# Kernel tuning notes

Hardware: AMD Instinct MI355X
Metric: run time of the kernel (lower is better)

Reference implementation:

```python
import jax, jax.numpy as jnp
import numpy as np

N_ING, N_DIR = 100000, 50000
E = 1000000
H, D = 4, 16          # heads, per-head dim
HID = H * D           # 64
LAT, COND = 32, 8
F_ING, F_DIR = 16, 8
OUT_ING = 16


def _han_edge(x_src, x_dst, att_s, att_d, edge_index, n_dst):
    # HANConv per-edge-type attention message passing.
    src, dst = edge_index[0], edge_index[1]
    a = jax.nn.leaky_relu(
        jnp.einsum('nhd,hd->nh', x_src, att_s)[src]
        + jnp.einsum('nhd,hd->nh', x_dst, att_d)[dst],
        negative_slope=0.2)                               # [E, H]
    amax = jax.ops.segment_max(a, dst, num_segments=n_dst)
    ex = jnp.exp(a - amax[dst])
    denom = jax.ops.segment_sum(ex, dst, num_segments=n_dst)
    alpha = ex / (denom[dst] + 1e-16)                     # PyG softmax eps
    out = jax.ops.segment_sum(x_src[src] * alpha[:, :, None], dst,
                              num_segments=n_dst)         # [n_dst, H, D]
    return jax.nn.relu(out.reshape(n_dst, HID))


def _group(outs, q, Wk, bk):
    # HANConv semantic-level attention across edge types.
    s = jnp.stack(outs)                                   # [T, N, HID]
    score = jnp.tanh(s @ Wk + bk).mean(axis=1) @ q        # [T]
    attn = jax.nn.softmax(score)
    return jnp.einsum('t,tnf->nf', attn, s)


def setup_inputs() -> dict:
    key = jax.random.key(0)
    ks = jax.random.split(key, 32)
    def ei(k, n_src, n_dst):
        k1, k2 = jax.random.split(k)
        return jnp.stack([jax.random.randint(k1, (E,), 0, n_src),
                          jax.random.randint(k2, (E,), 0, n_dst)]).astype(jnp.int64)
    s = 0.1
    inp = {
        'x_ing': jax.random.normal(ks[0], (N_ING, F_ING), jnp.float32),
        'x_dir': jax.random.normal(ks[1], (N_DIR, F_DIR), jnp.float32),
        'cond':  jax.random.normal(ks[2], (COND,), jnp.float32),
        'eps':   jax.random.normal(ks[3], (1, LAT), jnp.float32),
        'ei_cooc':     ei(ks[4], N_ING, N_DIR),
        'ei_used':     ei(ks[5], N_ING, N_DIR),
        'ei_contains': ei(ks[6], N_DIR, N_ING),
        'ei_pairs':    ei(ks[7], N_DIR, N_DIR),
        'ei_follows':  ei(ks[8], N_DIR, N_DIR),
        # node-type projections
        'W_pi': jax.random.normal(ks[9],  (F_ING, HID)) * s,
        'b_pi': jnp.zeros((HID,)),
        'W_pd': jax.random.normal(ks[10], (F_DIR, HID)) * s,
        'b_pd': jnp.zeros((HID,)),
        # semantic attention
        'Wk': jax.random.normal(ks[21], (HID, HID)) * s,
        'bk': jnp.zeros((HID,)),
        'q':  jax.random.normal(ks[22], (HID,)) * s,
        # VAE heads (input: 2*HID + COND)
        'W_mu': jax.random.normal(ks[23], (2 * HID + COND, LAT)) * s,
        'b_mu': jnp.zeros((LAT,)),
        'W_lv': jax.random.normal(ks[24], (2 * HID + COND, LAT)) * s,
        'b_lv': jnp.zeros((LAT,)),
        # decoder (fc1 is dead code in the original forward)
        'W_fc3': jax.random.normal(ks[25], (LAT, HID)) * s,
        'b_fc3': jnp.zeros((HID,)),
        'W_fc2': jax.random.normal(ks[26], (HID, OUT_ING)) * s,
        'b_fc2': jnp.zeros((OUT_ING,)),
    }
    for i, name in enumerate(['cooc', 'used', 'contains', 'pairs', 'follows']):
        inp[f'as_{name}'] = jax.random.normal(ks[11 + i], (H, D)) * s
        inp[f'ad_{name}'] = jax.random.normal(ks[16 + i], (H, D)) * s
    return inp


def reference(x_ing, x_dir, cond, eps,
              ei_cooc, ei_used, ei_contains, ei_pairs, ei_follows,
              W_pi, b_pi, W_pd, b_pd,
              as_cooc, ad_cooc, as_used, ad_used, as_contains, ad_contains,
              as_pairs, ad_pairs, as_follows, ad_follows,
              Wk, bk, q, W_mu, b_mu, W_lv, b_lv,
              W_fc3, b_fc3, W_fc2, b_fc2):
    # node-type projections -> [N, H, D]
    h_ing = (x_ing @ W_pi + b_pi).reshape(N_ING, H, D)
    h_dir = (x_dir @ W_pd + b_pd).reshape(N_DIR, H, D)

    o_cooc = _han_edge(h_ing, h_dir, as_cooc, ad_cooc, ei_cooc, N_DIR)
    o_used = _han_edge(h_ing, h_dir, as_used, ad_used, ei_used, N_DIR)
    o_cont = _han_edge(h_dir, h_ing, as_contains, ad_contains, ei_contains, N_ING)
    o_pair = _han_edge(h_dir, h_dir, as_pairs, ad_pairs, ei_pairs, N_DIR)
    o_foll = _han_edge(h_dir, h_dir, as_follows, ad_follows, ei_follows, N_DIR)

    out_ing = _group([o_cont], q, Wk, bk)                       # [N_ING, HID]
    out_dir = _group([o_cooc, o_used, o_pair, o_foll], q, Wk, bk)

    ingre_pool = out_ing.mean(axis=0, keepdims=True)            # [1, HID]
    direc_pool = out_dir.mean(axis=0, keepdims=True)
    graph_repr = jnp.concatenate([ingre_pool, direc_pool, cond[None]], axis=1)

    mu = graph_repr @ W_mu + b_mu
    logvar = graph_repr @ W_lv + b_lv
    z = mu + eps * jnp.exp(0.5 * logvar)

    # decoder: fc1 branch is overwritten in the original; effective path below
    recon = jnp.tanh(jax.nn.relu(z @ W_fc3 + b_fc3) @ W_fc2 + b_fc2)  # [1, OUT_ING]
    return recon, mu, logvar
```

## Files before the change

### kernel.cpp

```cpp
#include <hip/hip_runtime.h>
#include <hip/hip_fp16.h>
#include <math.h>

#define N_ING 100000
#define N_DIR 50000
#define NE    1000000
#define NDST_TOTAL 300000
#define NBUCK 4688
#define BA    16
#define NBK   (5 * BA)
#define I4PT  (NE / 4)
#define PB_ING 384
#define PB_DIR 192

typedef float v2f __attribute__((ext_vector_type(2)));

__global__ __launch_bounds__(256) void kA_kernel(
    const int* __restrict__ e0, const int* __restrict__ e1,
    const int* __restrict__ e2, const int* __restrict__ e3,
    const int* __restrict__ e4, int* __restrict__ blockcnt,
    const float* __restrict__ x_ing, const float* __restrict__ W_pi,
    const float* __restrict__ b_pi,
    const float* __restrict__ as_cooc, const float* __restrict__ as_used,
    const float* __restrict__ ad_contains,
    unsigned* __restrict__ h8_ing, __half* __restrict__ s_ing,
    const float* __restrict__ x_dir, const float* __restrict__ W_pd,
    const float* __restrict__ b_pd,
    const float* __restrict__ ad_cooc, const float* __restrict__ ad_used,
    const float* __restrict__ as_contains, const float* __restrict__ as_pairs,
    const float* __restrict__ ad_pairs, const float* __restrict__ as_follows,
    const float* __restrict__ ad_follows,
    unsigned* __restrict__ h8_dir, __half* __restrict__ s_dir)
{
    __shared__ int hist[NBUCK];
    __shared__ float sW[16 * 64];
    __shared__ float sbb[64];
    __shared__ float satt[7 * 64];
    __shared__ float sx[4][16];
    __shared__ float srow[4][64];

    const int bid = blockIdx.x;
    const int tid = threadIdx.x;
    if (bid < NBK) {
        const int type = bid / BA, blk = bid % BA;
        const int* ei = type == 0 ? e0 : type == 1 ? e1 : type == 2 ? e2
                      : type == 3 ? e3 : e4;
        const int base = type == 0 ? 0 : type == 1 ? 50000 : type == 2 ? 100000
                       : type == 3 ? 200000 : 250000;
        for (int i = tid; i < NBUCK; i += 256) hist[i] = 0;
        __syncthreads();
        const int4* d4 = (const int4*)(ei + NE);
        for (int i = blk * 256 + tid; i < I4PT; i += BA * 256) {
            int4 d = d4[i];
            atomicAdd(&hist[(base + d.x) >> 6], 1);
            atomicAdd(&hist[(base + d.y) >> 6], 1);
            atomicAdd(&hist[(base + d.z) >> 6], 1);
            atomicAdd(&hist[(base + d.w) >> 6], 1);
        }
        __syncthreads();
        int* row = blockcnt + (size_t)bid * NBUCK;
        for (int i = tid; i < NBUCK; i += 256) row[i] = hist[i];
    } else if (bid < NBK + PB_ING) {
        const int g = tid >> 6, t = tid & 63;
        for (int i = tid; i < 16 * 64; i += 256) sW[i] = W_pi[i];
        if (tid < 64) {
            sbb[tid] = b_pi[tid];
            satt[tid]       = as_cooc[tid];
            satt[64 + tid]  = as_used[tid];
            satt[128 + tid] = ad_contains[tid];
        }
        __syncthreads();
        for (int q = bid - NBK; q < N_ING / 4; q += PB_ING) {
            int n = q * 4 + g;
            if (t < 16) sx[g][t] = x_ing[(size_t)n * 16 + t];
            __syncthreads();
            float s = sbb[t];
#pragma unroll
            for (int i = 0; i < 16; ++i) s += sx[g][i] * sW[i * 64 + t];
            srow[g][t] = s;
            __syncthreads();
            if (t < 16) {
                int w0 = __builtin_amdgcn_cvt_pk_fp8_f32(srow[g][t * 4], srow[g][t * 4 + 1], 0, false);
                int w  = __builtin_amdgcn_cvt_pk_fp8_f32(srow[g][t * 4 + 2], srow[g][t * 4 + 3], w0, true);
                h8_ing[(size_t)n * 16 + t] = (unsigned)w;
            }
            if (t < 12) {
                int slot = t >> 2, hh = t & 3;
                float sc = 0.f;
#pragma unroll
                for (int d = 0; d < 16; ++d)
                    sc += srow[g][hh * 16 + d] * satt[slot * 64 + hh * 16 + d];
                s_ing[(size_t)n * 12 + t] = __float2half(sc);
            }
            __syncthreads();
        }
    } else {
        const int g = tid >> 6, t = tid & 63;
        for (int i = tid; i < 8 * 64; i += 256) sW[i] = W_pd[i];
        if (tid < 64) {
            sbb[tid] = b_pd[tid];
            satt[tid]        = ad_cooc[tid];
            satt[64  + tid]  = ad_used[tid];
            satt[128 + tid]  = as_contains[tid];
            satt[192 + tid]  = as_pairs[tid];
            satt[256 + tid]  = ad_pairs[tid];
            satt[320 + tid]  = as_follows[tid];
            satt[384 + tid]  = ad_follows[tid];
        }
        __syncthreads();
        for (int q = bid - NBK - PB_ING; q < N_DIR / 4; q += PB_DIR) {
            int n = q * 4 + g;
            if (t < 8) sx[g][t] = x_dir[(size_t)n * 8 + t];
            __syncthreads();
            float s = sbb[t];
#pragma unroll
            for (int i = 0; i < 8; ++i) s += sx[g][i] * sW[i * 64 + t];
            srow[g][t] = s;
            __syncthreads();
            if (t < 16) {
                int w0 = __builtin_amdgcn_cvt_pk_fp8_f32(srow[g][t * 4], srow[g][t * 4 + 1], 0, false);
                int w  = __builtin_amdgcn_cvt_pk_fp8_f32(srow[g][t * 4 + 2], srow[g][t * 4 + 3], w0, true);
                h8_dir[(size_t)n * 16 + t] = (unsigned)w;
            }
            if (t < 28) {
                int slot = t >> 2, hh = t & 3;
                float sc = 0.f;
#pragma unroll
                for (int d = 0; d < 16; ++d)
                    sc += srow[g][hh * 16 + d] * satt[slot * 64 + hh * 16 + d];
                s_dir[(size_t)n * 28 + t] = __float2half(sc);
            }
            __syncthreads();
        }
    }
}

__global__ __launch_bounds__(256) void k2_kernel(
    const int* __restrict__ blockcnt, int* __restrict__ blockbase,
    int* __restrict__ bbase, int* __restrict__ btot, int* __restrict__ cursor)
{
    __shared__ int part[4][64];
    __shared__ int tots[64];
    __shared__ int scn[64];
    __shared__ int bw;
    const int tid = threadIdx.x;
    const int kq = tid >> 6, bl = tid & 63;
    const int b = blockIdx.x * 64 + bl;
    const int K = NBK / 4;
    int ps = 0;
    if (b < NBUCK)
        for (int k = kq * K; k < kq * K + K; ++k)
            ps += blockcnt[(size_t)k * NBUCK + b];
    part[kq][bl] = ps;
    __syncthreads();
    if (tid < 64) {
        int t = part[0][tid] + part[1][tid] + part[2][tid] + part[3][tid];
        tots[tid] = t;
        scn[tid] = t;
    }
    __syncthreads();
    for (int off = 1; off < 64; off <<= 1) {
        int v = 0;
        if (tid < 64 && tid >= off) v = scn[tid - off];
        __syncthreads();
        if (tid < 64) scn[tid] += v;
        __syncthreads();
    }
    if (tid == 63) bw = atomicAdd(cursor, scn[63]);
    __syncthreads();
    if (b < NBUCK) {
        int bs = bw + scn[bl] - tots[bl];
        if (kq == 0) {
            bbase[b] = bs;
            btot[b] = tots[bl];
        }
        int run = bs;
        for (int q = 0; q < kq; ++q) run += part[q][bl];
        for (int k = kq * K; k < kq * K + K; ++k) {
            blockbase[(size_t)k * NBUCK + b] = run;
            run += blockcnt[(size_t)k * NBUCK + b];
        }
    }
}

__global__ __launch_bounds__(256) void k3_kernel(
    const int* __restrict__ e0, const int* __restrict__ e1,
    const int* __restrict__ e2, const int* __restrict__ e3,
    const int* __restrict__ e4, const int* __restrict__ blockbase,
    unsigned* __restrict__ bpair)
{
    __shared__ int cur[NBUCK];
    const int bid = blockIdx.x, tid = threadIdx.x;
    const int type = bid / BA, blk = bid % BA;
    const int* ei = type == 0 ? e0 : type == 1 ? e1 : type == 2 ? e2
                  : type == 3 ? e3 : e4;
    const int base = type == 0 ? 0 : type == 1 ? 50000 : type == 2 ? 100000
                   : type == 3 ? 200000 : 250000;
    const int* row = blockbase + (size_t)bid * NBUCK;
    for (int i = tid; i < NBUCK; i += 256) cur[i] = row[i];
    __syncthreads();
    const int4* s4 = (const int4*)ei;
    const int4* d4 = (const int4*)(ei + NE);
    for (int i = blk * 256 + tid; i < I4PT; i += BA * 256) {
        int4 s = s4[i];
        int4 d = d4[i];
        int g0 = base + d.x, g1 = base + d.y, g2 = base + d.z, g3 = base + d.w;
        int p0 = atomicAdd(&cur[g0 >> 6], 1);
        int p1 = atomicAdd(&cur[g1 >> 6], 1);
        int p2 = atomicAdd(&cur[g2 >> 6], 1);
        int p3 = atomicAdd(&cur[g3 >> 6], 1);
        bpair[p0] = ((unsigned)(g0 & 63) << 17) | (unsigned)s.x;
        bpair[p1] = ((unsigned)(g1 & 63) << 17) | (unsigned)s.y;
        bpair[p2] = ((unsigned)(g2 & 63) << 17) | (unsigned)s.z;
        bpair[p3] = ((unsigned)(g3 & 63) << 17) | (unsigned)s.w;
    }
}

__global__ __launch_bounds__(256) void k4_kernel(
    const unsigned* __restrict__ bpair, const int* __restrict__ bbase,
    const int* __restrict__ btot, int* __restrict__ perm,
    int* __restrict__ start, int* __restrict__ cnt)
{
    __shared__ int h[64], sc[64], cu[64];
    const int b = blockIdx.x, tid = threadIdx.x;
    const int jb = bbase[b], n = btot[b];
    if (tid < 64) h[tid] = 0;
    __syncthreads();
    for (int i = tid; i < n; i += 256)
        atomicAdd(&h[bpair[jb + i] >> 17], 1);
    __syncthreads();
    if (tid == 0) {
        int r = 0;
        for (int i = 0; i < 64; ++i) { sc[i] = r; cu[i] = r; r += h[i]; }
    }
    __syncthreads();
    if (tid < 64) {
        int dg = b * 64 + tid;
        if (dg < NDST_TOTAL) {
            start[dg] = jb + sc[tid];
            cnt[dg] = h[tid];
        }
    }
    for (int i = tid; i < n; i += 256) {
        unsigned p = bpair[jb + i];
        int pos = atomicAdd(&cu[p >> 17], 1);
        perm[jb + pos] = (int)(p & 0x1FFFF);
    }
}

__global__ __launch_bounds__(256) void agg_all_kernel(
    const int* __restrict__ perm, const int* __restrict__ start,
    const int* __restrict__ cnttot,
    const unsigned* __restrict__ h8_ing, const unsigned* __restrict__ h8_dir,
    const __half* __restrict__ s_ing, const __half* __restrict__ s_dir,
    const float* __restrict__ Wk, const float* __restrict__ bk,
    float* __restrict__ pool_ing, float* __restrict__ pool_dir,
    float* __restrict__ sem_dir)
{
    __shared__ float sWk[64 * 64];
    __shared__ float srow[4][64];
    __shared__ float sred[4][64];
    const int t = threadIdx.x & 63, w = threadIdx.x >> 6;
    const int g  = t >> 4;
    const int l4 = t & 15;
    const int hq = l4 >> 2;
    for (int i = threadIdx.x; i < 4096; i += 256) sWk[i] = Wk[i];
    const float bkf = bk[t];
    float p_ing = 0.f;
    float p0 = 0.f, p1 = 0.f, p2 = 0.f, p3 = 0.f;
    float m0 = 0.f, m1 = 0.f, m2 = 0.f, m3 = 0.f;
    __syncthreads();
    const int nwaves = gridDim.x * 4;
    for (int d = blockIdx.x * 4 + w; d < NDST_TOTAL; d += nwaves) {
        int type, ld;
        const __half *ssrc, *sdst;
        const unsigned* hsrc;
        int ss, soff, ds, doff;
        if (d < 50000)       { type = 0; ld = d;          ssrc = s_ing; ss = 12; soff = 0;  sdst = s_dir; ds = 28; doff = 0;  hsrc = h8_ing; }
        else if (d < 100000) { type = 1; ld = d - 50000;  ssrc = s_ing; ss = 12; soff = 4;  sdst = s_dir; ds = 28; doff = 4;  hsrc = h8_ing; }
        else if (d < 200000) { type = 2; ld = d - 100000; ssrc = s_dir; ss = 28; soff = 8;  sdst = s_ing; ds = 12; doff = 8;  hsrc = h8_dir; }
        else if (d < 250000) { type = 3; ld = d - 200000; ssrc = s_dir; ss = 28; soff = 12; sdst = s_dir; ds = 28; doff = 16; hsrc = h8_dir; }
        else                 { type = 4; ld = d - 250000; ssrc = s_dir; ss = 28; soff = 20; sdst = s_dir; ds = 28; doff = 24; hsrc = h8_dir; }
        float adst = __half2float(sdst[(size_t)ld * ds + doff + hq]);
        int jb = start[d], je = jb + cnttot[d];
        float4 acc = make_float4(0.f, 0.f, 0.f, 0.f);
        float dsum = 0.f;
        for (int j = jb; j < je; j += 8) {
            int j0 = j + g, j1 = j + 4 + g;
            bool v0 = j0 < je, v1 = j1 < je;
            int s0 = perm[v0 ? j0 : je - 1];
            int s1 = perm[v1 ? j1 : je - 1];
            float c0 = __half2float(ssrc[(size_t)s0 * ss + soff + hq]);
            float c1 = __half2float(ssrc[(size_t)s1 * ss + soff + hq]);
            unsigned u0 = hsrc[(size_t)s0 * 16 + l4];
            unsigned u1 = hsrc[(size_t)s1 * 16 + l4];
            float a0 = c0 + adst; a0 = a0 > 0.f ? a0 : 0.2f * a0;
            float a1 = c1 + adst; a1 = a1 > 0.f ? a1 : 0.2f * a1;
            float e0 = v0 ? __expf(a0) : 0.f;
            float e1 = v1 ? __expf(a1) : 0.f;
            dsum += e0 + e1;
            v2f lo0 = __builtin_amdgcn_cvt_pk_f32_fp8((int)u0, false);
            v2f hi0 = __builtin_amdgcn_cvt_pk_f32_fp8((int)u0, true);
            v2f lo1 = __builtin_amdgcn_cvt_pk_f32_fp8((int)u1, false);
            v2f hi1 = __builtin_amdgcn_cvt_pk_f32_fp8((int)u1, true);
            acc.x += lo0.x * e0 + lo1.x * e1;
            acc.y += lo0.y * e0 + lo1.y * e1;
            acc.z += hi0.x * e0 + hi1.x * e1;
            acc.w += hi0.y * e0 + hi1.y * e1;
        }
#pragma unroll
        for (int mask = 16; mask <= 32; mask <<= 1) {
            acc.x += __shfl_xor(acc.x, mask, 64);
            acc.y += __shfl_xor(acc.y, mask, 64);
            acc.z += __shfl_xor(acc.z, mask, 64);
            acc.w += __shfl_xor(acc.w, mask, 64);
            dsum  += __shfl_xor(dsum,  mask, 64);
        }
        float inv = 1.f / (dsum + 1e-16f);
        float4 v4 = make_float4(fmaxf(acc.x * inv, 0.f), fmaxf(acc.y * inv, 0.f),
                                fmaxf(acc.z * inv, 0.f), fmaxf(acc.w * inv, 0.f));
        if (g == 0) *(float4*)&srow[w][l4 * 4] = v4;
        float v = srow[w][t];
        if (type == 2) {
            p_ing += v;
        } else {
            float a2 = bkf;
#pragma unroll
            for (int k = 0; k < 64; ++k) a2 += srow[w][k] * sWk[k * 64 + t];
            float tv = tanhf(a2);
            if (type == 0)      { p0 += v; m0 += tv; }
            else if (type == 1) { p1 += v; m1 += tv; }
            else if (type == 3) { p2 += v; m2 += tv; }
            else                { p3 += v; m3 += tv; }
        }
    }
    float vals[9] = { p_ing, p0, p1, p2, p3, m0, m1, m2, m3 };
    float* outs[9] = { pool_ing, pool_dir, pool_dir + 64, pool_dir + 128,
                       pool_dir + 192, sem_dir, sem_dir + 64, sem_dir + 128,
                       sem_dir + 192 };
    for (int i = 0; i < 9; ++i) {
        __syncthreads();
        sred[w][t] = vals[i];
        __syncthreads();
        if (w == 0)
            atomicAdd(&outs[i][t], sred[0][t] + sred[1][t] + sred[2][t] + sred[3][t]);
    }
}

__global__ __launch_bounds__(64) void final_kernel(
    const float* __restrict__ pool_ing, const float* __restrict__ pool_dir,
    const float* __restrict__ sem_dir, const float* __restrict__ q,
    const float* __restrict__ cond, const float* __restrict__ eps,
    const float* __restrict__ W_mu, const float* __restrict__ b_mu,
    const float* __restrict__ W_lv, const float* __restrict__ b_lv,
    const float* __restrict__ W_fc3, const float* __restrict__ b_fc3,
    const float* __restrict__ W_fc2, const float* __restrict__ b_fc2,
    float* __restrict__ out)
{
    __shared__ float gr[136];
    __shared__ float sc[4], attn[4];
    __shared__ float z[32], hfc[64];
    int t = threadIdx.x;
    if (t < 4) {
        float s = 0.f;
        for (int f = 0; f < 64; ++f)
            s += (sem_dir[t * 64 + f] / (float)N_DIR) * q[f];
        sc[t] = s;
    }
    gr[t] = pool_ing[t] / (float)N_ING;
    __syncthreads();
    if (t == 0) {
        float m = fmaxf(fmaxf(sc[0], sc[1]), fmaxf(sc[2], sc[3]));
        float ssum = 0.f;
        for (int i = 0; i < 4; ++i) { attn[i] = expf(sc[i] - m); ssum += attn[i]; }
        for (int i = 0; i < 4; ++i) attn[i] /= ssum;
    }
    __syncthreads();
    {
        float v = 0.f;
        for (int tt = 0; tt < 4; ++tt)
            v += attn[tt] * (pool_dir[tt * 64 + t] / (float)N_DIR);
        gr[64 + t] = v;
    }
    if (t < 8) gr[128 + t] = cond[t];
    __syncthreads();
    if (t < 32) {
        float m = b_mu[t], lv = b_lv[t];
        for (int i = 0; i < 136; ++i) {
            float g = gr[i];
            m  += g * W_mu[i * 32 + t];
            lv += g * W_lv[i * 32 + t];
        }
        out[16 + t] = m;
        out[48 + t] = lv;
        z[t] = m + eps[t] * expf(0.5f * lv);
    }
    __syncthreads();
    {
        float v = b_fc3[t];
        for (int j = 0; j < 32; ++j) v += z[j] * W_fc3[j * 64 + t];
        hfc[t] = fmaxf(v, 0.f);
    }
    __syncthreads();
    if (t < 16) {
        float v = b_fc2[t];
        for (int f = 0; f < 64; ++f) v += hfc[f] * W_fc2[f * 16 + t];
        out[t] = tanhf(v);
    }
}

extern "C" void kernel_launch(void* const* d_in, const int* in_sizes, int n_in,
                              void* d_out, int out_size, void* d_ws, size_t ws_size,
                              hipStream_t stream) {
    const float* x_ing = (const float*)d_in[0];
    const float* x_dir = (const float*)d_in[1];
    const float* cond  = (const float*)d_in[2];
    const float* eps   = (const float*)d_in[3];
    const int* ei_cooc     = (const int*)d_in[4];
    const int* ei_used     = (const int*)d_in[5];
    const int* ei_contains = (const int*)d_in[6];
    const int* ei_pairs    = (const int*)d_in[7];
    const int* ei_follows  = (const int*)d_in[8];
    const float* W_pi = (const float*)d_in[9];
    const float* b_pi = (const float*)d_in[10];
    const float* W_pd = (const float*)d_in[11];
    const float* b_pd = (const float*)d_in[12];
    const float* Wk   = (const float*)d_in[13];
    const float* bk   = (const float*)d_in[14];
    const float* q    = (const float*)d_in[15];
    const float* W_mu = (const float*)d_in[16];
    const float* b_mu = (const float*)d_in[17];
    const float* W_lv = (const float*)d_in[18];
    const float* b_lv = (const float*)d_in[19];
    const float* W_fc3 = (const float*)d_in[20];
    const float* b_fc3 = (const float*)d_in[21];
    const float* W_fc2 = (const float*)d_in[22];
    const float* b_fc2 = (const float*)d_in[23];
    const float* as_cooc     = (const float*)d_in[24];
    const float* ad_cooc     = (const float*)d_in[25];
    const float* as_used     = (const float*)d_in[26];
    const float* ad_used     = (const float*)d_in[27];
    const float* as_contains = (const float*)d_in[28];
    const float* ad_contains = (const float*)d_in[29];
    const float* as_pairs    = (const float*)d_in[30];
    const float* ad_pairs    = (const float*)d_in[31];
    const float* as_follows  = (const float*)d_in[32];
    const float* ad_follows  = (const float*)d_in[33];

    unsigned* bpair = (unsigned*)d_ws;
    unsigned* h8_ing = bpair + (size_t)5 * NE;
    unsigned* h8_dir = h8_ing + (size_t)N_ING * 16;
    __half* s_ing = (__half*)(h8_dir + (size_t)N_DIR * 16);
    __half* s_dir = s_ing + (size_t)N_ING * 12;
    int*   perm  = (int*)(s_dir + (size_t)N_DIR * 28);
    int*   blockcnt  = perm + (size_t)5 * NE;
    int*   blockbase = blockcnt + (size_t)NBK * NBUCK;
    int*   bbase  = blockbase + (size_t)NBK * NBUCK;
    int*   btot   = bbase + NBUCK;
    int*   start  = btot + NBUCK;
    int*   cnt    = start + NDST_TOTAL;
    int*   cursor = cnt + NDST_TOTAL;
    float* pool_ing = (float*)(cursor + 1);
    float* pool_dir = pool_ing + 64;
    float* sem_dir  = pool_dir + 256;

    hipMemsetAsync(cursor, 0, (1 + 64 + 256 + 256) * sizeof(int), stream);

    kA_kernel<<<NBK + PB_ING + PB_DIR, 256, 0, stream>>>(
        ei_cooc, ei_used, ei_contains, ei_pairs, ei_follows, blockcnt,
        x_ing, W_pi, b_pi, as_cooc, as_used, ad_contains, h8_ing, s_ing,
        x_dir, W_pd, b_pd, ad_cooc, ad_used, as_contains, as_pairs, ad_pairs,
        as_follows, ad_follows, h8_dir, s_dir);

    k2_kernel<<<(NBUCK + 63) / 64, 256, 0, stream>>>(
        blockcnt, blockbase, bbase, btot, cursor);

    k3_kernel<<<NBK, 256, 0, stream>>>(
        ei_cooc, ei_used, ei_contains, ei_pairs, ei_follows, blockbase, bpair);

    k4_kernel<<<NBUCK, 256, 0, stream>>>(bpair, bbase, btot, perm, start, cnt);

    agg_all_kernel<<<2048, 256, 0, stream>>>(
        perm, start, cnt, h8_ing, h8_dir, s_ing, s_dir, Wk, bk,
        pool_ing, pool_dir, sem_dir);

    final_kernel<<<1, 64, 0, stream>>>(
        pool_ing, pool_dir, sem_dir, q, cond, eps,
        W_mu, b_mu, W_lv, b_lv, W_fc3, b_fc3, W_fc2, b_fc2, (float*)d_out);
}
```

Baseline: 520.4 us.

## Privatize per-wave bucket histograms, cache Wk in registers, broadcast row via readlane

Doubles the bucket granularity constant BA. In the bucket-sort kernel, each wave gets its own shared histogram and cursor array, which cuts atomic contention, and per-destination counts are derived from prefix differences. In the aggregation kernel, each lane keeps its Wk column in 64 registers and broadcasts the row value with readlane, replacing the shared Wk tile and the LDS reads in the semantic projection. This frees LDS and a barrier, but raises VGPR pressure and may lower occupancy.

```diff
diff --git a/kernel.cpp b/kernel.cpp
--- a/kernel.cpp
+++ b/kernel.cpp
@@ -7,7 +7,7 @@
 #define NE    1000000
 #define NDST_TOTAL 300000
 #define NBUCK 4688
-#define BA    16
+#define BA    32
 #define NBK   (5 * BA)
 #define I4PT  (NE / 4)
 #define PB_ING 384
@@ -221,29 +221,41 @@
     const int* __restrict__ btot, int* __restrict__ perm,
     int* __restrict__ start, int* __restrict__ cnt)
 {
-    __shared__ int h[64], sc[64], cu[64];
+    __shared__ int hw[4][64];
+    __shared__ int sc[64];
+    __shared__ int cuw[4][64];
     const int b = blockIdx.x, tid = threadIdx.x;
+    const int w = tid >> 6;
     const int jb = bbase[b], n = btot[b];
-    if (tid < 64) h[tid] = 0;
+    if (tid < 256) { hw[tid >> 6][tid & 63] = 0; }
     __syncthreads();
     for (int i = tid; i < n; i += 256)
-        atomicAdd(&h[bpair[jb + i] >> 17], 1);
+        atomicAdd(&hw[w][bpair[jb + i] >> 17], 1);
     __syncthreads();
     if (tid == 0) {
         int r = 0;
-        for (int i = 0; i < 64; ++i) { sc[i] = r; cu[i] = r; r += h[i]; }
+        for (int i = 0; i < 64; ++i) {
+            int h0 = hw[0][i], h1 = hw[1][i], h2 = hw[2][i], h3 = hw[3][i];
+            sc[i] = r;
+            cuw[0][i] = r;
+            cuw[1][i] = r + h0;
+            cuw[2][i] = r + h0 + h1;
+            cuw[3][i] = r + h0 + h1 + h2;
+            r += h0 + h1 + h2 + h3;
+        }
     }
     __syncthreads();
     if (tid < 64) {
         int dg = b * 64 + tid;
         if (dg < NDST_TOTAL) {
             start[dg] = jb + sc[tid];
-            cnt[dg] = h[tid];
+            int nx = (tid < 63) ? sc[tid + 1] : n;
+            cnt[dg] = nx - sc[tid];
         }
     }
     for (int i = tid; i < n; i += 256) {
         unsigned p = bpair[jb + i];
-        int pos = atomicAdd(&cu[p >> 17], 1);
+        int pos = atomicAdd(&cuw[w][p >> 17], 1);
         perm[jb + pos] = (int)(p & 0x1FFFF);
     }
 }
@@ -257,19 +269,19 @@
     float* __restrict__ pool_ing, float* __restrict__ pool_dir,
     float* __restrict__ sem_dir)
 {
-    __shared__ float sWk[64 * 64];
     __shared__ float srow[4][64];
     __shared__ float sred[4][64];
     const int t = threadIdx.x & 63, w = threadIdx.x >> 6;
     const int g  = t >> 4;
     const int l4 = t & 15;
     const int hq = l4 >> 2;
-    for (int i = threadIdx.x; i < 4096; i += 256) sWk[i] = Wk[i];
+    float wkc[64];
+#pragma unroll
+    for (int k = 0; k < 64; ++k) wkc[k] = Wk[k * 64 + t];
     const float bkf = bk[t];
     float p_ing = 0.f;
     float p0 = 0.f, p1 = 0.f, p2 = 0.f, p3 = 0.f;
     float m0 = 0.f, m1 = 0.f, m2 = 0.f, m3 = 0.f;
-    __syncthreads();
     const int nwaves = gridDim.x * 4;
     for (int d = blockIdx.x * 4 + w; d < NDST_TOTAL; d += nwaves) {
         int type, ld;
@@ -326,7 +338,8 @@
         } else {
             float a2 = bkf;
 #pragma unroll
-            for (int k = 0; k < 64; ++k) a2 += srow[w][k] * sWk[k * 64 + t];
+            for (int k = 0; k < 64; ++k)
+                a2 += __int_as_float(__builtin_amdgcn_readlane(__float_as_int(v), k)) * wkc[k];
             float tv = tanhf(a2);
             if (type == 0)      { p0 += v; m0 += tv; }
             else if (type == 1) { p1 += v; m1 += tv; }
```

New measurement: 591.8 us. 1.14x slower.
